# Performance work log

Measured on AMD Instinct MI355X. Metric: run time of the kernel, lower is better.

## Reference

```python
import jax, jax.numpy as jnp
import numpy as np

EMBED_DIM = 2048
HEAD_DIM = 128            # __init__ head_dim arg
HALF = HEAD_DIM // 2      # internal self.head_dim = 64
NH2 = EMBED_DIM // HALF   # 32 q/k heads
H = NH2 // 2              # 16 differential heads
DEPTH = 12
LAMBDA_INIT = 0.8 - 0.6 * float(np.exp(-0.3 * DEPTH))
SCALING = HEAD_DIM ** (-0.5)   # source divides scores by this (== *sqrt(head_dim))
BATCH, SEQ = 1, 2048
EPS = 1e-5


def setup_inputs() -> dict:
    key = jax.random.key(0)
    ks = jax.random.split(key, 10)
    wstd = 0.25 / float(np.sqrt(EMBED_DIM))  # keep logits moderate despite *sqrt(head_dim)
    return {
        "x": jax.random.normal(ks[0], (BATCH, SEQ, EMBED_DIM), jnp.float32),
        "wq": jax.random.normal(ks[1], (EMBED_DIM, EMBED_DIM), jnp.float32) * wstd,
        "wk": jax.random.normal(ks[2], (EMBED_DIM, EMBED_DIM), jnp.float32) * wstd,
        "wv": jax.random.normal(ks[3], (EMBED_DIM, EMBED_DIM), jnp.float32) * wstd,
        "wout": jax.random.normal(ks[4], (EMBED_DIM, EMBED_DIM), jnp.float32) * wstd,
        "lambda_q1": jax.random.normal(ks[5], (HALF,), jnp.float32) * 0.1,
        "lambda_q2": jax.random.normal(ks[6], (HALF,), jnp.float32) * 0.1,
        "lambda_k1": jax.random.normal(ks[7], (HALF,), jnp.float32) * 0.1,
        "lambda_k2": jax.random.normal(ks[8], (HALF,), jnp.float32) * 0.1,
        "subln_weight": jnp.ones((2 * HALF,), jnp.float32),
    }


def _rope_tables(t, dim):
    # precompute_freqs_cis: freqs = 1/theta^(arange(0,dim,2)/dim); angles = outer(t, freqs)
    inv = 1.0 / (10000.0 ** (np.arange(0, dim, 2)[: dim // 2].astype(np.float64) / dim))
    ang = np.outer(np.arange(t), inv)
    return jnp.asarray(np.cos(ang), jnp.float32), jnp.asarray(np.sin(ang), jnp.float32)


def _apply_rope(x, cos, sin):
    # x: [b, t, h, d]; interleaved (even, odd) pairs form complex numbers
    xr, xi = x[..., 0::2], x[..., 1::2]
    c = cos[None, :, None, :]
    s = sin[None, :, None, :]
    out = jnp.stack([xr * c - xi * s, xr * s + xi * c], axis=-1)
    return out.reshape(x.shape)


def reference(x, wq, wk, wv, wout, lambda_q1, lambda_q2, lambda_k1, lambda_k2, subln_weight):
    b, t, e = x.shape
    # nn.Linear(bias=False): y = x @ W^T
    q = (x @ wq.T).reshape(b, t, NH2, HALF)
    k = (x @ wk.T).reshape(b, t, NH2, HALF)
    v = (x @ wv.T).reshape(b, t, H, 2 * HALF)  # intended DIFF-attn layout
    cos, sin = _rope_tables(t, HALF)
    q = _apply_rope(q, cos, sin)
    k = _apply_rope(k, cos, sin)
    q = q.transpose(0, 2, 1, 3)  # [b, 2H, t, HALF]
    k = k.transpose(0, 2, 1, 3)
    v = v.transpose(0, 2, 1, 3)  # [b, H, t, 2*HALF]
    # source: attn_weights = qk / scaling  (scaling = head_dim**-0.5 -> multiply by sqrt(head_dim))
    scores = jnp.einsum('bhtd,bhsd->bhts', q, k) / SCALING
    # default attn_mask = triu(zeros) == all zeros -> no masking applied
    probs = jax.nn.softmax(scores, axis=-1)
    lam1 = jnp.exp(jnp.sum(lambda_q1 * lambda_k1))
    lam2 = jnp.exp(jnp.sum(lambda_q2 * lambda_k2))
    lam = lam1 - lam2 + LAMBDA_INIT
    probs = probs.reshape(b, H, 2, t, t)
    diff = probs[:, :, 0] - lam * probs[:, :, 1]        # [b, H, t, t]
    attn = jnp.einsum('bhts,bhsd->bhtd', diff, v)        # [b, H, t, 2*HALF]
    # RMSNorm(2*HALF, eps=1e-5)
    attn = attn * jax.lax.rsqrt(jnp.mean(attn * attn, axis=-1, keepdims=True) + EPS)
    attn = attn * subln_weight
    attn = attn.transpose(0, 2, 1, 3).reshape(b, t, e)
    return attn @ wout.T
```

## Files before the change

### kernel.cpp

```cpp
#include <hip/hip_runtime.h>
#include <math.h>

#define SEQ 2048
#define EMB 2048

typedef _Float16 f16;
typedef unsigned short ushort_t;
typedef __attribute__((ext_vector_type(2))) _Float16 f16x2;
typedef __attribute__((ext_vector_type(4))) _Float16 f16x4;
typedef __attribute__((ext_vector_type(8))) _Float16 f16x8;
typedef __attribute__((ext_vector_type(4))) float f32x4;
typedef __attribute__((ext_vector_type(16))) float f32x16;
typedef __attribute__((ext_vector_type(8))) short bf16x8;
typedef __attribute__((ext_vector_type(4))) unsigned short us4;
typedef __attribute__((ext_vector_type(8))) unsigned short us8;
typedef __attribute__((ext_vector_type(4))) unsigned int uint4v;

__device__ __forceinline__ void gload16(const void* g, void* l) {
  __builtin_amdgcn_global_load_lds((const __attribute__((address_space(1))) unsigned int*)g,
                                   (__attribute__((address_space(3))) unsigned int*)l, 16, 0, 0);
}

__device__ __forceinline__ ushort_t f32_to_bf16(float f) {
  unsigned int u = __builtin_bit_cast(unsigned int, f);
  u += 0x7FFFu + ((u >> 16) & 1u);
  return (ushort_t)(u >> 16);
}

__device__ __forceinline__ unsigned cvt_pk_bf16_2(float lo, float hi) {
  unsigned r;
  asm("v_cvt_pk_bf16_f32 %0, %1, %2" : "=v"(r) : "v"(lo), "v"(hi));
  return r;
}

__global__ __launch_bounds__(256) void cvt5_kernel(const float* __restrict__ i0,
                                                   const float* __restrict__ i1,
                                                   const float* __restrict__ i2,
                                                   const float* __restrict__ i3,
                                                   const float* __restrict__ i4,
                                                   f16* __restrict__ o0, f16* __restrict__ o1,
                                                   f16* __restrict__ o2, f16* __restrict__ o3,
                                                   f16* __restrict__ o4) {
  int b = blockIdx.x;
  int z = b >> 12;
  const float* in = (z == 0) ? i0 : (z == 1) ? i1 : (z == 2) ? i2 : (z == 3) ? i3 : i4;
  f16* out = (z == 0) ? o0 : (z == 1) ? o1 : (z == 2) ? o2 : (z == 3) ? o3 : o4;
  int i = ((b & 4095) * 256 + threadIdx.x) * 4;
  f32x4 v = *(const f32x4*)(in + i);
  *(f16x4*)(out + i) = __builtin_convertvector(v, f16x4);
}

__global__ __launch_bounds__(256) void rope_table_kernel(float* __restrict__ cosT,
                                                         float* __restrict__ sinT) {
  int id = blockIdx.x * 256 + threadIdx.x;
  int t = id >> 5, i = id & 31;
  double inv = pow(10000.0, -(double)i / 32.0);
  double ang = (double)t * inv;
  cosT[id] = (float)cos(ang);
  sinT[id] = (float)sin(ang);
}

__global__ __launch_bounds__(256, 3) void proj_gemm_kernel(
    const f16* __restrict__ A, const f16* __restrict__ B0, const f16* __restrict__ B1,
    const f16* __restrict__ B2, const float* __restrict__ cosT, const float* __restrict__ sinT,
    f16* __restrict__ qout, f16* __restrict__ kout, ushort_t* __restrict__ vtout) {
  const int z = blockIdx.z;
  const f16* __restrict__ B = (z == 0) ? B0 : ((z == 1) ? B1 : B2);
  __shared__ f16 As[128 * 32];
  __shared__ f16 Bs[128 * 32];
  const int tid = threadIdx.x;
  const int wave = tid >> 6, lane = tid & 63;
  const int l16 = lane & 15, quad = lane >> 4;
  const int wm = (wave >> 1) << 6, wn = (wave & 1) << 6;
  const int bm = blockIdx.y << 7, bn = blockIdx.x << 7;

  const int swg = ((lane & 3) ^ ((lane >> 3) & 3)) * 8;
  const f16* Ag = A + (size_t)(bm + wave * 32 + (lane >> 2)) * EMB + swg;
  const f16* Bg = B + (size_t)(bn + wave * 32 + (lane >> 2)) * EMB + swg;
  f16* Asl = &As[wave * 1024 + lane * 8];
  f16* Bsl = &Bs[wave * 1024 + lane * 8];

  const int swr = (quad ^ ((l16 >> 1) & 3)) * 8;
  int aoff[4], boff[4];
#pragma unroll
  for (int i = 0; i < 4; i++) {
    aoff[i] = (wm + i * 16 + l16) * 32 + swr;
    boff[i] = (wn + i * 16 + l16) * 32 + swr;
  }

  f32x4 acc[4][4];
#pragma unroll
  for (int i = 0; i < 4; i++)
#pragma unroll
    for (int j = 0; j < 4; j++) acc[i][j] = (f32x4){0.f, 0.f, 0.f, 0.f};

  for (int k0 = 0; k0 < EMB; k0 += 32) {
    __syncthreads();
    gload16(Ag + k0, Asl);
    gload16(Ag + (size_t)16 * EMB + k0, Asl + 512);
    gload16(Bg + k0, Bsl);
    gload16(Bg + (size_t)16 * EMB + k0, Bsl + 512);
    __syncthreads();
    f16x8 af[4], bf[4];
#pragma unroll
    for (int mi = 0; mi < 4; mi++) af[mi] = *(const f16x8*)&As[aoff[mi]];
#pragma unroll
    for (int ni = 0; ni < 4; ni++) bf[ni] = *(const f16x8*)&Bs[boff[ni]];
#pragma unroll
    for (int mi = 0; mi < 4; mi++)
#pragma unroll
      for (int ni = 0; ni < 4; ni++)
        acc[mi][ni] = __builtin_amdgcn_mfma_f32_16x16x32_f16(af[mi], bf[ni], acc[mi][ni], 0, 0, 0);
  }

  if (z == 2) {
#pragma unroll
    for (int mi = 0; mi < 4; mi++) {
#pragma unroll
      for (int ni = 0; ni < 4; ni++) {
        int row0 = bm + wm + mi * 16 + quad * 4;
        int col = bn + wn + ni * 16 + l16;
        us4 o;
#pragma unroll
        for (int rg = 0; rg < 4; rg++) o[rg] = f32_to_bf16(acc[mi][ni][rg]);
        int hidx = col >> 7, d = col & 127, t = row0;
        size_t idx = ((((size_t)hidx * 32 + (t >> 6)) * 4 + ((t >> 4) & 3)) * 4 + (d >> 5)) * 512 +
                     (((t >> 3) & 1) * 32 + (d & 31)) * 8 + (t & 7);
        *(us4*)&vtout[idx] = o;
      }
    }
  } else {
    f16* Co = (z == 0) ? qout : kout;
    const float scale = (z == 0) ? 16.3222307f : 1.0f;
#pragma unroll
    for (int mi = 0; mi < 4; mi++) {
#pragma unroll
      for (int ni = 0; ni < 4; ni++) {
        int row0 = bm + wm + mi * 16 + quad * 4;
        int col = bn + wn + ni * 16 + l16;
        int i_r = (col & 63) >> 1;
        int odd = col & 1;
        int hidx = col >> 7, d = col & 127;
#pragma unroll
        for (int rg = 0; rg < 4; rg++) {
          int t = row0 + rg;
          float c = cosT[(t << 5) + i_r] * scale;
          float s = sinT[(t << 5) + i_r] * scale;
          float own = acc[mi][ni][rg];
          float other = __shfl_xor(own, 1);
          float xr = odd ? other : own;
          float xi = odd ? own : other;
          float outv = odd ? (xr * s + xi * c) : (xr * c - xi * s);
          size_t idx = ((size_t)((hidx * 64 + (t >> 5)) * 8 + (d >> 4))) * 512 +
                       ((t & 31) + ((d >> 3) & 1) * 32) * 8 + (d & 7);
          Co[idx] = (f16)outv;
        }
      }
    }
  }
}

__global__ __launch_bounds__(256, 2) void out_gemm_kernel(const f16* __restrict__ A,
                                                          const f16* __restrict__ B,
                                                          float* __restrict__ C) {
  __shared__ f16 As[128 * 32];
  __shared__ f16 Bs[64 * 32];
  const int tid = threadIdx.x;
  const int wave = tid >> 6, lane = tid & 63;
  const int l16 = lane & 15, quad = lane >> 4;
  const int wm = (wave >> 1) << 6, wn = (wave & 1) << 5;
  const int bm = blockIdx.y << 7, bn = blockIdx.x << 6;

  const int swg = ((lane & 3) ^ ((lane >> 3) & 3)) * 8;
  const f16* Ag = A + (size_t)(bm + wave * 32 + (lane >> 2)) * EMB + swg;
  const f16* Bg = B + (size_t)(bn + wave * 16 + (lane >> 2)) * EMB + swg;
  f16* Asl = &As[wave * 1024 + lane * 8];
  f16* Bsl = &Bs[wave * 512 + lane * 8];

  const int swr = (quad ^ ((l16 >> 1) & 3)) * 8;
  int aoff[4], boff[2];
#pragma unroll
  for (int i = 0; i < 4; i++) aoff[i] = (wm + i * 16 + l16) * 32 + swr;
#pragma unroll
  for (int i = 0; i < 2; i++) boff[i] = (wn + i * 16 + l16) * 32 + swr;

  f32x4 acc[4][2];
#pragma unroll
  for (int i = 0; i < 4; i++)
#pragma unroll
    for (int j = 0; j < 2; j++) acc[i][j] = (f32x4){0.f, 0.f, 0.f, 0.f};

  for (int k0 = 0; k0 < EMB; k0 += 32) {
    __syncthreads();
    gload16(Ag + k0, Asl);
    gload16(Ag + (size_t)16 * EMB + k0, Asl + 512);
    gload16(Bg + k0, Bsl);
    __syncthreads();
    f16x8 af[4], bf[2];
#pragma unroll
    for (int mi = 0; mi < 4; mi++) af[mi] = *(const f16x8*)&As[aoff[mi]];
#pragma unroll
    for (int ni = 0; ni < 2; ni++) bf[ni] = *(const f16x8*)&Bs[boff[ni]];
#pragma unroll
    for (int mi = 0; mi < 4; mi++)
#pragma unroll
      for (int ni = 0; ni < 2; ni++)
        acc[mi][ni] = __builtin_amdgcn_mfma_f32_16x16x32_f16(af[mi], bf[ni], acc[mi][ni], 0, 0, 0);
  }

#pragma unroll
  for (int mi = 0; mi < 4; mi++) {
#pragma unroll
    for (int ni = 0; ni < 2; ni++) {
      int row0 = bm + wm + mi * 16 + quad * 4;
      int col = bn + wn + ni * 16 + l16;
#pragma unroll
      for (int rg = 0; rg < 4; rg++)
        C[(size_t)(row0 + rg) * EMB + col] = acc[mi][ni][rg];
    }
  }
}

__global__ __launch_bounds__(256, 2) void diff_attn_v11(
    const f16* __restrict__ qbT, const f16* __restrict__ kbT, const ushort_t* __restrict__ vbT,
    const float* __restrict__ lq1, const float* __restrict__ lq2,
    const float* __restrict__ lk1, const float* __restrict__ lk2,
    const float* __restrict__ subw, f16* __restrict__ attnb) {
  const int h = blockIdx.x;
  const int qblk = blockIdx.y;
  const int tid = threadIdx.x;
  const int wave = tid >> 6, lane = tid & 63;
  const int l32 = lane & 31, hi = lane >> 5;
  const int hh = wave >> 1, qs = wave & 1;

  __shared__ float Obuf[8192];

  const int qrow0 = qblk * 64 + qs * 32;
  f16x8 qf[4];
  {
    const f16* qT = qbT + ((size_t)((h * 64 + qblk * 2 + qs) * 8 + hh * 4)) * 512 + lane * 8;
#pragma unroll
    for (int c = 0; c < 4; c++) qf[c] = *(const f16x8*)(qT + c * 512);
  }

  f32x16 O[4];
#pragma unroll
  for (int dt = 0; dt < 4; dt++)
#pragma unroll
    for (int s2 = 0; s2 < 16; s2++) O[dt][s2] = 0.f;
  float lsum = 0.f;

  const f16* kT = kbT + ((size_t)(h * 64) * 8 + hh * 4) * 512 + lane * 8;
  const ushort_t* vT = vbT + (size_t)h * 262144 + lane * 8;

  auto loadK = [&](f16x8(&kr)[4], int it) {
    const f16* p = kT + (size_t)it * 4096;
#pragma unroll
    for (int c = 0; c < 4; c++) kr[c] = *(const f16x8*)(p + c * 512);
  };
  auto loadV = [&](us8(&vr)[8], int it) {
    const ushort_t* p = vT + (size_t)it * 4096;
#pragma unroll
    for (int T = 0; T < 8; T++) vr[T] = *(const us8*)(p + T * 512);
  };

  auto compute = [&](const f16x8(&kr)[4], const us8(&vr)[8]) {
    f32x16 acc;
#pragma unroll
    for (int s2 = 0; s2 < 16; s2++) acc[s2] = -28.8539008f;
#pragma unroll
    for (int c = 0; c < 4; c++)
      acc = __builtin_amdgcn_mfma_f32_32x32x16_f16(kr[c], qf[c], acc, 0, 0, 0);
    float p[16];
#pragma unroll
    for (int s2 = 0; s2 < 16; s2++) p[s2] = __builtin_exp2f(acc[s2]);
    lsum += (((p[0] + p[1]) + (p[2] + p[3])) + ((p[4] + p[5]) + (p[6] + p[7]))) +
            (((p[8] + p[9]) + (p[10] + p[11])) + ((p[12] + p[13]) + (p[14] + p[15])));
    bf16x8 pf[2];
#pragma unroll
    for (int c2 = 0; c2 < 2; c2++) {
      unsigned w0 = cvt_pk_bf16_2(p[8 * c2 + 0], p[8 * c2 + 1]);
      unsigned w1 = cvt_pk_bf16_2(p[8 * c2 + 2], p[8 * c2 + 3]);
      unsigned w2 = cvt_pk_bf16_2(p[8 * c2 + 4], p[8 * c2 + 5]);
      unsigned w3 = cvt_pk_bf16_2(p[8 * c2 + 6], p[8 * c2 + 7]);
      asm("v_permlane32_swap_b32 %0, %1" : "+v"(w0), "+v"(w2));
      asm("v_permlane32_swap_b32 %0, %1" : "+v"(w1), "+v"(w3));
      uint4v pw;
      pw.x = w0; pw.y = w1; pw.z = w2; pw.w = w3;
      pf[c2] = __builtin_bit_cast(bf16x8, pw);
    }
    __builtin_amdgcn_s_setprio(1);
#pragma unroll
    for (int c2 = 0; c2 < 2; c2++) {
#pragma unroll
      for (int dt = 0; dt < 4; dt++) {
        bf16x8 vf = __builtin_bit_cast(bf16x8, vr[c2 * 4 + dt]);
        O[dt] = __builtin_amdgcn_mfma_f32_32x32x16_bf16(vf, pf[c2], O[dt], 0, 0, 0);
      }
    }
    __builtin_amdgcn_s_setprio(0);
  };

  f16x8 kA[4], kB[4];
  us8 vA[8], vB[8];
  loadK(kA, 0);
  loadV(vA, 0);
  loadK(kB, 1);
  loadV(vB, 1);
  for (int it = 0; it < 64; it += 2) {
    compute(kA, vA);
    if (it + 2 < 64) {
      loadK(kA, it + 2);
      loadV(vA, it + 2);
    }
    compute(kB, vB);
    if (it + 3 < 64) {
      loadK(kB, it + 3);
      loadV(vB, it + 3);
    }
  }

  float d1 = 0.f, d2 = 0.f;
  for (int i = 0; i < 64; i++) {
    d1 += lq1[i] * lk1[i];
    d2 += lq2[i] * lk2[i];
  }
  const float lam = __expf(d1) - __expf(d2) + 0.783605767f;

  float s = lsum + __shfl_xor(lsum, 32);
  const float inv = (hh == 0) ? (1.f / s) : (lam / s);

  if (hh == 1) {
#pragma unroll
    for (int dt = 0; dt < 4; dt++)
#pragma unroll
      for (int rq = 0; rq < 4; rq++) {
        f32x4 v;
#pragma unroll
        for (int rg = 0; rg < 4; rg++) v[rg] = O[dt][rq * 4 + rg] * inv;
        *(f32x4*)&Obuf[(((qs * 4 + dt) * 4 + rq) * 64 + lane) * 4] = v;
      }
  }
  __syncthreads();
  if (hh == 0) {
    float a[4][16];
    float ms = 0.f;
#pragma unroll
    for (int dt = 0; dt < 4; dt++)
#pragma unroll
      for (int rq = 0; rq < 4; rq++) {
        f32x4 o1 = *(const f32x4*)&Obuf[(((qs * 4 + dt) * 4 + rq) * 64 + lane) * 4];
#pragma unroll
        for (int rg = 0; rg < 4; rg++) {
          float v = O[dt][rq * 4 + rg] * inv - o1[rg];
          a[dt][rq * 4 + rg] = v;
          ms += v * v;
        }
      }
    ms += __shfl_xor(ms, 32);
    const float rms = rsqrtf(ms * (1.f / 128.f) + 1e-5f);
    const int t_g = qrow0 + l32;
#pragma unroll
    for (int dt = 0; dt < 4; dt++)
#pragma unroll
      for (int rq = 0; rq < 4; rq++) {
        f32x4 sw = *(const f32x4*)(subw + dt * 32 + rq * 8 + hi * 4);
        f16x4 o;
#pragma unroll
        for (int rg = 0; rg < 4; rg++) o[rg] = (f16)(a[dt][rq * 4 + rg] * rms * sw[rg]);
        *(f16x4*)(attnb + (size_t)t_g * EMB + h * 128 + dt * 32 + rq * 8 + hi * 4) = o;
      }
  }
}

extern "C" void kernel_launch(void* const* d_in, const int* in_sizes, int n_in,
                              void* d_out, int out_size, void* d_ws, size_t ws_size,
                              hipStream_t stream) {
  const float* x    = (const float*)d_in[0];
  const float* wq   = (const float*)d_in[1];
  const float* wk   = (const float*)d_in[2];
  const float* wv   = (const float*)d_in[3];
  const float* wout = (const float*)d_in[4];
  const float* lq1  = (const float*)d_in[5];
  const float* lq2  = (const float*)d_in[6];
  const float* lk1  = (const float*)d_in[7];
  const float* lk2  = (const float*)d_in[8];
  const float* subw = (const float*)d_in[9];
  float* out = (float*)d_out;

  char* ws = (char*)d_ws;
  const size_t MB = 1024 * 1024;
  f16* xb    = (f16*)(ws + 0 * MB);
  f16* wqb   = (f16*)(ws + 8 * MB);
  f16* wkb   = (f16*)(ws + 16 * MB);
  f16* wvb   = (f16*)(ws + 24 * MB);
  f16* woutb = (f16*)(ws + 32 * MB);
  f16* qbT   = (f16*)(ws + 40 * MB);
  f16* kbT   = (f16*)(ws + 48 * MB);
  ushort_t* vbT = (ushort_t*)(ws + 56 * MB);
  f16* attnb = (f16*)(ws + 64 * MB);
  float* cosT = (float*)(ws + 72 * MB);
  float* sinT = (float*)(ws + 72 * MB + 262144);

  dim3 b256(256);
  cvt5_kernel<<<5 * 4096, b256, 0, stream>>>(x, wq, wk, wv, wout, xb, wqb, wkb, wvb, woutb);
  rope_table_kernel<<<256, b256, 0, stream>>>(cosT, sinT);

  proj_gemm_kernel<<<dim3(16, 16, 3), b256, 0, stream>>>(xb, wqb, wkb, wvb, cosT, sinT, qbT, kbT,
                                                         vbT);

  diff_attn_v11<<<dim3(16, 32), b256, 0, stream>>>(qbT, kbT, vbT, lq1, lq2, lk1, lk2, subw,
                                                   attnb);

  out_gemm_kernel<<<dim3(32, 16), b256, 0, stream>>>(attnb, woutb, out);
}
```

Before: 296.0 us.

## Split attention key range across waves and double grid size

Each block now handles 32 query rows instead of 64, and its two wave pairs split the key sequence into even and odd tiles. Partial row sums and outputs are merged through shared memory. The grid doubles to 1024 blocks and launch bounds rise to 4 blocks per CU, aiming at better occupancy and load balance on the many CUs. The price is extra syncthreads, LDS traffic for the reduction, and reloading Q and K/V per block.

```diff
diff --git a/kernel.cpp b/kernel.cpp
--- a/kernel.cpp
+++ b/kernel.cpp
@@ -221,7 +221,7 @@
   }
 }
 
-__global__ __launch_bounds__(256, 2) void diff_attn_v11(
+__global__ __launch_bounds__(256, 4) void diff_attn_v12(
     const f16* __restrict__ qbT, const f16* __restrict__ kbT, const ushort_t* __restrict__ vbT,
     const float* __restrict__ lq1, const float* __restrict__ lq2,
     const float* __restrict__ lk1, const float* __restrict__ lk2,
@@ -231,14 +231,15 @@
   const int tid = threadIdx.x;
   const int wave = tid >> 6, lane = tid & 63;
   const int l32 = lane & 31, hi = lane >> 5;
-  const int hh = wave >> 1, qs = wave & 1;
-
-  __shared__ float Obuf[8192];
-
-  const int qrow0 = qblk * 64 + qs * 32;
+  const int hh = wave >> 1, ks = wave & 1;
+
+  __shared__ float OB[8192];
+  __shared__ float lsb[2][2][32];
+
+  const int qrow0 = qblk * 32;
   f16x8 qf[4];
   {
-    const f16* qT = qbT + ((size_t)((h * 64 + qblk * 2 + qs) * 8 + hh * 4)) * 512 + lane * 8;
+    const f16* qT = qbT + ((size_t)((h * 64 + qblk) * 8 + hh * 4)) * 512 + lane * 8;
 #pragma unroll
     for (int c = 0; c < 4; c++) qf[c] = *(const f16x8*)(qT + c * 512);
   }
@@ -303,20 +304,20 @@
 
   f16x8 kA[4], kB[4];
   us8 vA[8], vB[8];
-  loadK(kA, 0);
-  loadV(vA, 0);
-  loadK(kB, 1);
-  loadV(vB, 1);
-  for (int it = 0; it < 64; it += 2) {
+  loadK(kA, ks);
+  loadV(vA, ks);
+  loadK(kB, ks + 2);
+  loadV(vB, ks + 2);
+  for (int si = 0; si < 32; si += 2) {
     compute(kA, vA);
-    if (it + 2 < 64) {
-      loadK(kA, it + 2);
-      loadV(vA, it + 2);
+    if (si + 2 < 32) {
+      loadK(kA, ks + 2 * (si + 2));
+      loadV(vA, ks + 2 * (si + 2));
     }
     compute(kB, vB);
-    if (it + 3 < 64) {
-      loadK(kB, it + 3);
-      loadV(vB, it + 3);
+    if (si + 3 < 32) {
+      loadK(kB, ks + 2 * (si + 3));
+      loadV(vB, ks + 2 * (si + 3));
     }
   }
 
@@ -327,32 +328,65 @@
   }
   const float lam = __expf(d1) - __expf(d2) + 0.783605767f;
 
-  float s = lsum + __shfl_xor(lsum, 32);
-  const float inv = (hh == 0) ? (1.f / s) : (lam / s);
-
-  if (hh == 1) {
+  const float sp = lsum + __shfl_xor(lsum, 32);
+  if (hi == 0) lsb[hh][ks][l32] = sp;
+  __syncthreads();
+  const float den = lsb[hh][0][l32] + lsb[hh][1][l32];
+  const float inv = (hh == 0) ? (1.f / den) : (lam / den);
+
+#pragma unroll
+  for (int dt = 0; dt < 4; dt++)
+#pragma unroll
+    for (int s2 = 0; s2 < 16; s2++) O[dt][s2] *= inv;
+
+  auto obIdx = [&](int hhR, int dt, int rq) { return (((hhR * 4 + dt) * 4 + rq) * 64 + lane) * 4; };
+
+  if (ks == 1) {
 #pragma unroll
     for (int dt = 0; dt < 4; dt++)
 #pragma unroll
       for (int rq = 0; rq < 4; rq++) {
         f32x4 v;
 #pragma unroll
-        for (int rg = 0; rg < 4; rg++) v[rg] = O[dt][rq * 4 + rg] * inv;
-        *(f32x4*)&Obuf[(((qs * 4 + dt) * 4 + rq) * 64 + lane) * 4] = v;
+        for (int rg = 0; rg < 4; rg++) v[rg] = O[dt][rq * 4 + rg];
+        *(f32x4*)&OB[obIdx(hh, dt, rq)] = v;
       }
   }
   __syncthreads();
-  if (hh == 0) {
+  if (ks == 0) {
+#pragma unroll
+    for (int dt = 0; dt < 4; dt++)
+#pragma unroll
+      for (int rq = 0; rq < 4; rq++) {
+        f32x4 v1 = *(const f32x4*)&OB[obIdx(hh, dt, rq)];
+#pragma unroll
+        for (int rg = 0; rg < 4; rg++) O[dt][rq * 4 + rg] += v1[rg];
+      }
+  }
+  __syncthreads();
+  if (ks == 0 && hh == 1) {
+#pragma unroll
+    for (int dt = 0; dt < 4; dt++)
+#pragma unroll
+      for (int rq = 0; rq < 4; rq++) {
+        f32x4 v;
+#pragma unroll
+        for (int rg = 0; rg < 4; rg++) v[rg] = O[dt][rq * 4 + rg];
+        *(f32x4*)&OB[obIdx(1, dt, rq)] = v;
+      }
+  }
+  __syncthreads();
+  if (ks == 0 && hh == 0) {
     float a[4][16];
     float ms = 0.f;
 #pragma unroll
     for (int dt = 0; dt < 4; dt++)
 #pragma unroll
       for (int rq = 0; rq < 4; rq++) {
-        f32x4 o1 = *(const f32x4*)&Obuf[(((qs * 4 + dt) * 4 + rq) * 64 + lane) * 4];
+        f32x4 o1 = *(const f32x4*)&OB[obIdx(1, dt, rq)];
 #pragma unroll
         for (int rg = 0; rg < 4; rg++) {
-          float v = O[dt][rq * 4 + rg] * inv - o1[rg];
+          float v = O[dt][rq * 4 + rg] - o1[rg];
           a[dt][rq * 4 + rg] = v;
           ms += v * v;
         }
@@ -409,7 +443,7 @@
   proj_gemm_kernel<<<dim3(16, 16, 3), b256, 0, stream>>>(xb, wqb, wkb, wvb, cosT, sinT, qbT, kbT,
                                                          vbT);
 
-  diff_attn_v11<<<dim3(16, 32), b256, 0, stream>>>(qbT, kbT, vbT, lq1, lq2, lk1, lk2, subw,
+  diff_attn_v12<<<dim3(16, 64), b256, 0, stream>>>(qbT, kbT, vbT, lq1, lq2, lk1, lk2, subw,
                                                    attnb);
 
   out_gemm_kernel<<<dim3(32, 16), b256, 0, stream>>>(attnb, woutb, out);
```

New measurement: 750.2 us. +153.4%, slower.

## Software-pipeline QK and PV stages and compute row sums via MFMA ones

Applied to the files above, without the earlier changes.

Restructures the attention loop so the QK^T MFMAs for the next key block are issued before the exp/pack and PV MFMAs of the current block, with K and V loads staggered to overlap. The softmax denominator is now accumulated through an extra MFMA against a ones matrix instead of scalar adds plus a cross-lane shuffle. This aims to hide exp and conversion latency behind matrix work and remove VALU reductions. In exchange it adds more MFMA work, more live accumulator registers, and sums the bf16-rounded probabilities rather than the fp32 ones.

```diff
diff --git a/kernel.cpp b/kernel.cpp
--- a/kernel.cpp
+++ b/kernel.cpp
@@ -221,7 +221,7 @@
   }
 }
 
-__global__ __launch_bounds__(256, 2) void diff_attn_v11(
+__global__ __launch_bounds__(256, 2) void diff_attn_v13(
     const f16* __restrict__ qbT, const f16* __restrict__ kbT, const ushort_t* __restrict__ vbT,
     const float* __restrict__ lq1, const float* __restrict__ lq2,
     const float* __restrict__ lk1, const float* __restrict__ lk2,
@@ -244,11 +244,25 @@
   }
 
   f32x16 O[4];
+  f32x16 Osum;
 #pragma unroll
   for (int dt = 0; dt < 4; dt++)
 #pragma unroll
     for (int s2 = 0; s2 < 16; s2++) O[dt][s2] = 0.f;
-  float lsum = 0.f;
+#pragma unroll
+  for (int s2 = 0; s2 < 16; s2++) Osum[s2] = 0.f;
+
+  f32x16 biasC;
+#pragma unroll
+  for (int s2 = 0; s2 < 16; s2++) biasC[s2] = -28.8539008f;
+
+  bf16x8 ones;
+  {
+    us8 o;
+#pragma unroll
+    for (int j = 0; j < 8; j++) o[j] = 0x3F80;
+    ones = __builtin_bit_cast(bf16x8, o);
+  }
 
   const f16* kT = kbT + ((size_t)(h * 64) * 8 + hh * 4) * 512 + lane * 8;
   const ushort_t* vT = vbT + (size_t)h * 262144 + lane * 8;
@@ -264,19 +278,18 @@
     for (int T = 0; T < 8; T++) vr[T] = *(const us8*)(p + T * 512);
   };
 
-  auto compute = [&](const f16x8(&kr)[4], const us8(&vr)[8]) {
-    f32x16 acc;
-#pragma unroll
-    for (int s2 = 0; s2 < 16; s2++) acc[s2] = -28.8539008f;
-#pragma unroll
-    for (int c = 0; c < 4; c++)
+  auto qk4 = [&](const f16x8(&kr)[4]) {
+    f32x16 acc = __builtin_amdgcn_mfma_f32_32x32x16_f16(kr[0], qf[0], biasC, 0, 0, 0);
+#pragma unroll
+    for (int c = 1; c < 4; c++)
       acc = __builtin_amdgcn_mfma_f32_32x32x16_f16(kr[c], qf[c], acc, 0, 0, 0);
+    return acc;
+  };
+
+  auto exppack = [&](const f32x16& acc, bf16x8(&pf)[2]) {
     float p[16];
 #pragma unroll
     for (int s2 = 0; s2 < 16; s2++) p[s2] = __builtin_exp2f(acc[s2]);
-    lsum += (((p[0] + p[1]) + (p[2] + p[3])) + ((p[4] + p[5]) + (p[6] + p[7]))) +
-            (((p[8] + p[9]) + (p[10] + p[11])) + ((p[12] + p[13]) + (p[14] + p[15])));
-    bf16x8 pf[2];
 #pragma unroll
     for (int c2 = 0; c2 < 2; c2++) {
       unsigned w0 = cvt_pk_bf16_2(p[8 * c2 + 0], p[8 * c2 + 1]);
@@ -289,9 +302,13 @@
       pw.x = w0; pw.y = w1; pw.z = w2; pw.w = w3;
       pf[c2] = __builtin_bit_cast(bf16x8, pw);
     }
+  };
+
+  auto pv = [&](const us8(&vr)[8], const bf16x8(&pf)[2]) {
     __builtin_amdgcn_s_setprio(1);
 #pragma unroll
     for (int c2 = 0; c2 < 2; c2++) {
+      Osum = __builtin_amdgcn_mfma_f32_32x32x16_bf16(ones, pf[c2], Osum, 0, 0, 0);
 #pragma unroll
       for (int dt = 0; dt < 4; dt++) {
         bf16x8 vf = __builtin_bit_cast(bf16x8, vr[c2 * 4 + dt]);
@@ -307,17 +324,22 @@
   loadV(vA, 0);
   loadK(kB, 1);
   loadV(vB, 1);
+  f32x16 acc_e = qk4(kA);
+  loadK(kA, 2);
+
   for (int it = 0; it < 64; it += 2) {
-    compute(kA, vA);
-    if (it + 2 < 64) {
-      loadK(kA, it + 2);
-      loadV(vA, it + 2);
-    }
-    compute(kB, vB);
-    if (it + 3 < 64) {
-      loadK(kB, it + 3);
-      loadV(vB, it + 3);
-    }
+    f32x16 acc_o = qk4(kB);
+    loadK(kB, (it + 3 < 64) ? it + 3 : 63);
+    bf16x8 pf[2];
+    exppack(acc_e, pf);
+    pv(vA, pf);
+    loadV(vA, (it + 2 < 64) ? it + 2 : 63);
+    acc_e = qk4(kA);
+    loadK(kA, (it + 4 < 64) ? it + 4 : 63);
+    bf16x8 pg[2];
+    exppack(acc_o, pg);
+    pv(vB, pg);
+    loadV(vB, (it + 3 < 64) ? it + 3 : 63);
   }
 
   float d1 = 0.f, d2 = 0.f;
@@ -327,8 +349,7 @@
   }
   const float lam = __expf(d1) - __expf(d2) + 0.783605767f;
 
-  float s = lsum + __shfl_xor(lsum, 32);
-  const float inv = (hh == 0) ? (1.f / s) : (lam / s);
+  const float inv = (hh == 0) ? (1.f / Osum[0]) : (lam / Osum[0]);
 
   if (hh == 1) {
 #pragma unroll
@@ -409,7 +430,7 @@
   proj_gemm_kernel<<<dim3(16, 16, 3), b256, 0, stream>>>(xb, wqb, wkb, wvb, cosT, sinT, qbT, kbT,
                                                          vbT);
 
-  diff_attn_v11<<<dim3(16, 32), b256, 0, stream>>>(qbT, kbT, vbT, lq1, lq2, lk1, lk2, subw,
+  diff_attn_v13<<<dim3(16, 32), b256, 0, stream>>>(qbT, kbT, vbT, lq1, lq2, lk1, lk2, subw,
                                                    attnb);
 
   out_gemm_kernel<<<dim3(32, 16), b256, 0, stream>>>(attnb, woutb, out);
```

Measured after the change: 327.5 us. 1.11x slower.
